# Optimization experiments

Hardware: AMD Instinct MI355X
Metric: run time of the kernel (lower is better)

## Reference

```python
import jax, jax.numpy as jnp
import numpy as np

BCE_W, AMP_W, SMOOTH_W = 1.0, 0.5, 0.3
BIG = 1e30  # finite sentinel for masked min/max (avoids inf-inf NaNs)


def setup_inputs() -> dict:
    key = jax.random.key(0)
    k1, k2, k3 = jax.random.split(key, 3)
    B, L = 128, 100000
    signals = jax.random.normal(k1, (B, 1, L), dtype=jnp.float32)
    predictions = jax.random.normal(k2, (B, L, 1), dtype=jnp.float32)
    targets = jax.random.uniform(k3, (B, L, 1), dtype=jnp.float32)
    return {"signals": signals, "predictions": predictions, "targets": targets}


def _window_amp(mask, s, idx, L):
    # mask: [B, L] bool; s: [B, L] signal. Amplitude of s over [min_idx, max_idx].
    lo = jnp.min(jnp.where(mask, idx, L), axis=1)    # [B]
    hi = jnp.max(jnp.where(mask, idx, -1), axis=1)   # [B]
    w = (idx[None, :] >= lo[:, None]) & (idx[None, :] <= hi[:, None])  # [B, L]
    amp = jnp.max(jnp.where(w, s, -BIG), axis=1) - jnp.min(jnp.where(w, s, BIG), axis=1)
    return amp, jnp.any(mask, axis=1)


def reference(signals, predictions, targets):
    # predictions/targets: [B, L, 1] (3D path of the torch module)
    p, t = predictions, targets
    pred_sigmoid = jax.nn.sigmoid(p)
    # BCEWithLogitsLoss (mean), numerically stable
    bce_loss = jnp.mean(jnp.maximum(p, 0.0) - p * t + jnp.log1p(jnp.exp(-jnp.abs(p))))

    B, L = signals.shape[0], signals.shape[2]
    s = signals[:, 0, :]                              # [B, L]
    idx = jnp.arange(L)

    true_amp, t_has = _window_amp(t[:, :, 0] > 0.5, s, idx, L)
    pred_amp, p_has = _window_amp(pred_sigmoid[:, :, 0] > 0.5, s, idx, L)
    valid = t_has & p_has

    d = jnp.abs(true_amp - pred_amp)
    per = jnp.where(true_amp > 1e-6, d / (true_amp + 1e-6), d)
    amp_loss = jnp.sum(jnp.where(valid, per, 0.0)) / B

    # smoothness: mean |diff(pred_sigmoid, axis=1)|; L >= 2 so never empty
    smoothness_loss = jnp.mean(jnp.abs(pred_sigmoid[:, 1:, :] - pred_sigmoid[:, :-1, :]))

    return BCE_W * bce_loss + AMP_W * amp_loss + SMOOTH_W * smoothness_loss
```

## Files before the change

### kernel.cpp

```cpp
#include <hip/hip_runtime.h>
#include <math.h>
#include <float.h>

#define BATCH 128
#define LEN   100000
#define CHUNK 5000
#define SEGS  (LEN / CHUNK)
#define VPS   (CHUNK / 4)
#define THREADS 512
#define NG    3

struct WS {
    int*   lt_tab; int* ht_tab; int* lp_tab; int* hp_tab;
    float* bce_blk; float* sm_blk;
    float* cmin; float* cmax;
    float* wmn; float* wmx;
};

static inline WS ws_layout(void* d_ws) {
    WS w;
    w.lt_tab  = (int*)d_ws;
    w.ht_tab  = w.lt_tab + BATCH * SEGS;
    w.lp_tab  = w.ht_tab + BATCH * SEGS;
    w.hp_tab  = w.lp_tab + BATCH * SEGS;
    w.bce_blk = (float*)(w.hp_tab + BATCH * SEGS);
    w.sm_blk  = w.bce_blk + BATCH * SEGS;
    w.cmin    = w.sm_blk  + BATCH * SEGS;
    w.cmax    = w.cmin    + BATCH * SEGS;
    w.wmn     = w.cmax    + BATCH * SEGS;
    w.wmx     = w.wmn     + 2 * BATCH;
    return w;
}


__global__ __launch_bounds__(THREADS) void k_main(
        const float* __restrict__ sig,
        const float* __restrict__ pred,
        const float* __restrict__ targ,
        int* __restrict__ lt_tab, int* __restrict__ ht_tab,
        int* __restrict__ lp_tab, int* __restrict__ hp_tab,
        float* __restrict__ bce_blk, float* __restrict__ sm_blk,
        float* __restrict__ cmin_tab, float* __restrict__ cmax_tab) {
    const int b   = blockIdx.y;
    const int seg = blockIdx.x;
    const int tid = threadIdx.x;
    const size_t row = (size_t)b * LEN;
    const float* prow = pred + row;
    const float* trow = targ + row;
    const float* srow = sig  + row;
    const int seg0 = seg * CHUNK;
    const bool g2 = (tid < (VPS - 2 * THREADS));

    float4 pv[NG], tv[NG], sv[NG];
    #pragma unroll
    for (int k = 0; k < NG; ++k) {
        if (k < NG - 1 || g2) {
            const int l0 = seg0 + (tid + k * THREADS) * 4;
            pv[k] = *reinterpret_cast<const float4*>(prow + l0);
            tv[k] = *reinterpret_cast<const float4*>(trow + l0);
            sv[k] = *reinterpret_cast<const float4*>(srow + l0);
        }
    }

    float bce = 0.0f, sm = 0.0f;
    float cmn = FLT_MAX, cmx = -FLT_MAX;
    unsigned tmask = 0u, pmask = 0u;

    #pragma unroll
    for (int k = 0; k < NG; ++k) {
        if (k == NG - 1 && !g2) continue;
        const float4 p4 = pv[k];
        const float4 t4 = tv[k];
        const float4 s4 = sv[k];
        const int l0 = seg0 + (tid + k * THREADS) * 4;
        float sg0, sg1, sg2, sg3;
        #define ONE_ELEM(pp, tt, ss, sgv, BIT) { \
            const float ap = fabsf(pp); \
            const float ee = __expf(-ap); \
            const float zz = 1.0f + ee; \
            const float rr = __builtin_amdgcn_rcpf(zz); \
            bce += fmaxf(pp, 0.0f) - (pp) * (tt) + __logf(zz); \
            sgv = ((pp) >= 0.0f) ? rr : ee * rr; \
            tmask |= ((tt) > 0.5f) ? (1u << (BIT)) : 0u; \
            pmask |= ((pp) > 0.0f) ? (1u << (BIT)) : 0u; \
            cmn = fminf(cmn, (ss)); cmx = fmaxf(cmx, (ss)); }
        ONE_ELEM(p4.x, t4.x, s4.x, sg0, 4 * k + 0)
        ONE_ELEM(p4.y, t4.y, s4.y, sg1, 4 * k + 1)
        ONE_ELEM(p4.z, t4.z, s4.z, sg2, 4 * k + 2)
        ONE_ELEM(p4.w, t4.w, s4.w, sg3, 4 * k + 3)
        #undef ONE_ELEM
        sm += fabsf(sg1 - sg0) + fabsf(sg2 - sg1) + fabsf(sg3 - sg2);
        const float prev3 = __shfl_up(sg3, 1);
        if ((tid & 63) == 0) {
            if (l0 > 0) {
                const float pp = prow[l0 - 1];
                const float ee = __expf(-fabsf(pp));
                const float rr = __builtin_amdgcn_rcpf(1.0f + ee);
                const float sp = (pp >= 0.0f) ? rr : ee * rr;
                sm += fabsf(sg0 - sp);
            }
        } else {
            sm += fabsf(sg0 - prev3);
        }
    }

    int lt = LEN, ht = -1, lp = LEN, hp = -1;
    if (tmask) {
        const int f = __ffs(tmask) - 1;
        const int h = 31 - __clz((int)tmask);
        lt = seg0 + (tid + (f >> 2) * THREADS) * 4 + (f & 3);
        ht = seg0 + (tid + (h >> 2) * THREADS) * 4 + (h & 3);
    }
    if (pmask) {
        const int f = __ffs(pmask) - 1;
        const int h = 31 - __clz((int)pmask);
        lp = seg0 + (tid + (f >> 2) * THREADS) * 4 + (f & 3);
        hp = seg0 + (tid + (h >> 2) * THREADS) * 4 + (h & 3);
    }

    #pragma unroll
    for (int o = 32; o > 0; o >>= 1) {
        bce += __shfl_xor(bce, o);
        sm  += __shfl_xor(sm,  o);
        cmn  = fminf(cmn, __shfl_xor(cmn, o));
        cmx  = fmaxf(cmx, __shfl_xor(cmx, o));
        lt   = min(lt, __shfl_xor(lt, o));
        ht   = max(ht, __shfl_xor(ht, o));
        lp   = min(lp, __shfl_xor(lp, o));
        hp   = max(hp, __shfl_xor(hp, o));
    }

    __shared__ float s_bce[8], s_sm[8], s_mn[8], s_mx[8];
    __shared__ int   s_lt[8], s_ht[8], s_lp[8], s_hp[8];
    const int w = tid >> 6, lane = tid & 63;
    if (lane == 0) {
        s_bce[w] = bce; s_sm[w] = sm; s_mn[w] = cmn; s_mx[w] = cmx;
        s_lt[w] = lt; s_ht[w] = ht; s_lp[w] = lp; s_hp[w] = hp;
    }
    __syncthreads();
    if (tid == 0) {
        float B = 0.0f, S = 0.0f, MN = FLT_MAX, MX = -FLT_MAX;
        int LT = LEN, HT = -1, LP = LEN, HP = -1;
        #pragma unroll
        for (int i = 0; i < 8; ++i) {
            B += s_bce[i]; S += s_sm[i];
            MN = fminf(MN, s_mn[i]); MX = fmaxf(MX, s_mx[i]);
            LT = min(LT, s_lt[i]); HT = max(HT, s_ht[i]);
            LP = min(LP, s_lp[i]); HP = max(HP, s_hp[i]);
        }
        const int e = b * SEGS + seg;
        bce_blk[e] = B; sm_blk[e] = S;
        cmin_tab[e] = MN; cmax_tab[e] = MX;
        lt_tab[e] = LT; ht_tab[e] = HT;
        lp_tab[e] = LP; hp_tab[e] = HP;
    }
}


__global__ __launch_bounds__(THREADS) void k_rows(
        const float* __restrict__ sig,
        const int* __restrict__ lt_tab, const int* __restrict__ ht_tab,
        const int* __restrict__ lp_tab, const int* __restrict__ hp_tab,
        const float* __restrict__ cmin_tab, const float* __restrict__ cmax_tab,
        float* __restrict__ wmn, float* __restrict__ wmx) {
    const int b     = blockIdx.x;
    const int which = blockIdx.y;
    const int tid   = threadIdx.x;
    const int* lo_tab = which ? lp_tab : lt_tab;
    const int* hi_tab = which ? hp_tab : ht_tab;

    int lo = LEN, hi = -1;
    if (tid < SEGS) { lo = lo_tab[b * SEGS + tid]; hi = hi_tab[b * SEGS + tid]; }
    #pragma unroll
    for (int o = 32; o > 0; o >>= 1) {
        lo = min(lo, __shfl_xor(lo, o));
        hi = max(hi, __shfl_xor(hi, o));
    }
    __shared__ int s_lo, s_hi;
    if (tid == 0) { s_lo = lo; s_hi = hi; }
    __syncthreads();
    lo = s_lo; hi = s_hi;

    float mn = FLT_MAX, mx = -FLT_MAX;
    if (lo < LEN) {
        const float* srow = sig + (size_t)b * LEN;
        const int cl = lo / CHUNK, ch = hi / CHUNK;
        const int e1 = (cl == ch) ? hi : cl * CHUNK + CHUNK - 1;
        for (int l = lo + tid; l <= e1; l += THREADS) {
            const float x = srow[l]; mn = fminf(mn, x); mx = fmaxf(mx, x);
        }
        if (ch > cl) {
            for (int l = ch * CHUNK + tid; l <= hi; l += THREADS) {
                const float x = srow[l]; mn = fminf(mn, x); mx = fmaxf(mx, x);
            }
            const float* cmin_row = cmin_tab + b * SEGS;
            const float* cmax_row = cmax_tab + b * SEGS;
            for (int c = cl + 1 + tid; c < ch; c += THREADS) {
                mn = fminf(mn, cmin_row[c]); mx = fmaxf(mx, cmax_row[c]);
            }
        }
    }
    #pragma unroll
    for (int o = 32; o > 0; o >>= 1) {
        mn = fminf(mn, __shfl_xor(mn, o));
        mx = fmaxf(mx, __shfl_xor(mx, o));
    }
    __shared__ float sh_mn[8], sh_mx[8];
    const int w = tid >> 6, lane = tid & 63;
    if (lane == 0) { sh_mn[w] = mn; sh_mx[w] = mx; }
    __syncthreads();
    if (tid == 0) {
        float MN = FLT_MAX, MX = -FLT_MAX;
        #pragma unroll
        for (int i = 0; i < 8; ++i) {
            MN = fminf(MN, sh_mn[i]); MX = fmaxf(MX, sh_mx[i]);
        }
        if (lo >= LEN) { MN = 1e30f; MX = -1e30f; }
        wmn[which * BATCH + b] = MN;
        wmx[which * BATCH + b] = MX;
    }
}


__global__ void k_combine(const float* __restrict__ bce_blk,
                          const float* __restrict__ sm_blk,
                          const float* __restrict__ wmn,
                          const float* __restrict__ wmx,
                          float* __restrict__ out) {
    const int tid = threadIdx.x;
    float acc_b = 0.0f, acc_s = 0.0f, acc_a = 0.0f;
    for (int i = tid; i < BATCH * SEGS; i += 256) { acc_b += bce_blk[i]; acc_s += sm_blk[i]; }
    if (tid < BATCH) {
        const float tmn = wmn[tid],          tmx = wmx[tid];
        const float pmn = wmn[BATCH + tid],  pmx = wmx[BATCH + tid];
        if (tmx >= tmn && pmx >= pmn) {
            const float ta = tmx - tmn;
            const float pa = pmx - pmn;
            const float d  = fabsf(ta - pa);
            acc_a = (ta > 1e-6f) ? d / (ta + 1e-6f) : d;
        }
    }
    #pragma unroll
    for (int o = 32; o > 0; o >>= 1) {
        acc_b += __shfl_xor(acc_b, o);
        acc_s += __shfl_xor(acc_s, o);
        acc_a += __shfl_xor(acc_a, o);
    }
    __shared__ float sb[4], ss[4], sa[4];
    const int w = tid >> 6, lane = tid & 63;
    if (lane == 0) { sb[w] = acc_b; ss[w] = acc_s; sa[w] = acc_a; }
    __syncthreads();
    if (tid == 0) {
        const double B = (double)(sb[0] + sb[1] + sb[2] + sb[3]);
        const double S = (double)(ss[0] + ss[1] + ss[2] + ss[3]);
        const double A = (double)(sa[0] + sa[1] + sa[2] + sa[3]);
        const double bce = B / ((double)BATCH * (double)LEN);
        const double smo = S / ((double)BATCH * (double)(LEN - 1));
        const double amp = A / (double)BATCH;
        out[0] = (float)(1.0 * bce + 0.5 * amp + 0.3 * smo);
    }
}


extern "C" void kernel_launch(void* const* d_in, const int* in_sizes, int n_in,
                              void* d_out, int out_size, void* d_ws, size_t ws_size,
                              hipStream_t stream) {
    const float* signals = (const float*)d_in[0];
    const float* preds   = (const float*)d_in[1];
    const float* targs   = (const float*)d_in[2];
    float* out = (float*)d_out;
    WS w = ws_layout(d_ws);

    dim3 gm(SEGS, BATCH);
    k_main<<<gm, THREADS, 0, stream>>>(signals, preds, targs,
                                       w.lt_tab, w.ht_tab, w.lp_tab, w.hp_tab,
                                       w.bce_blk, w.sm_blk, w.cmin, w.cmax);

    dim3 gr(BATCH, 2);
    k_rows<<<gr, THREADS, 0, stream>>>(signals,
                                       w.lt_tab, w.ht_tab, w.lp_tab, w.hp_tab,
                                       w.cmin, w.cmax, w.wmn, w.wmx);

    k_combine<<<1, 256, 0, stream>>>(w.bce_blk, w.sm_blk, w.wmn, w.wmx, out);
}
```

Baseline: 43.29 us.

## Use fewer larger blocks per row with per-stripe min/max tables

The main kernel now uses 8 blocks per row, each covering 12500 elements over 7 strided iterations, instead of 20 blocks of 5000. Each iteration does its load and compute immediately rather than preloading all groups into registers. Each block records a signal min/max per 2048-element stripe, so the window kernel only rescans the partial boundary stripes instead of whole 5000-element chunks. The grid drops from 2560 to 1024 blocks and the boundary scans get shorter, at the cost of less memory-level parallelism per thread and a 1024-block grid that may underfill the GPU.

```diff
diff --git a/kernel.cpp b/kernel.cpp
--- a/kernel.cpp
+++ b/kernel.cpp
@@ -4,11 +4,17 @@
 
 #define BATCH 128
 #define LEN   100000
-#define CHUNK 5000
-#define SEGS  (LEN / CHUNK)
-#define VPS   (CHUNK / 4)
-#define THREADS 512
-#define NG    3
+#define BPR   8
+#define BCHUNK (LEN / BPR)
+#define BVEC  (BCHUNK / 4)
+#define T     512
+#define NG    7
+#define TAILV (BVEC - (NG - 1) * T)
+#define NST   7
+#define STRE  (T * 4)
+#define TAILE (TAILV * 4)
+#define NSEG  (BATCH * BPR)
+#define NSTR  (NSEG * NST)
 
 struct WS {
     int*   lt_tab; int* ht_tab; int* lp_tab; int* hp_tab;
@@ -20,20 +26,20 @@
 static inline WS ws_layout(void* d_ws) {
     WS w;
     w.lt_tab  = (int*)d_ws;
-    w.ht_tab  = w.lt_tab + BATCH * SEGS;
-    w.lp_tab  = w.ht_tab + BATCH * SEGS;
-    w.hp_tab  = w.lp_tab + BATCH * SEGS;
-    w.bce_blk = (float*)(w.hp_tab + BATCH * SEGS);
-    w.sm_blk  = w.bce_blk + BATCH * SEGS;
-    w.cmin    = w.sm_blk  + BATCH * SEGS;
-    w.cmax    = w.cmin    + BATCH * SEGS;
-    w.wmn     = w.cmax    + BATCH * SEGS;
+    w.ht_tab  = w.lt_tab + NSEG;
+    w.lp_tab  = w.ht_tab + NSEG;
+    w.hp_tab  = w.lp_tab + NSEG;
+    w.bce_blk = (float*)(w.hp_tab + NSEG);
+    w.sm_blk  = w.bce_blk + NSEG;
+    w.cmin    = w.sm_blk  + NSEG;
+    w.cmax    = w.cmin    + NSTR;
+    w.wmn     = w.cmax    + NSTR;
     w.wmx     = w.wmn     + 2 * BATCH;
     return w;
 }
 
 
-__global__ __launch_bounds__(THREADS) void k_main(
+__global__ __launch_bounds__(T, 8) void k_main(
         const float* __restrict__ sig,
         const float* __restrict__ pred,
         const float* __restrict__ targ,
@@ -42,122 +48,140 @@
         float* __restrict__ bce_blk, float* __restrict__ sm_blk,
         float* __restrict__ cmin_tab, float* __restrict__ cmax_tab) {
     const int b   = blockIdx.y;
-    const int seg = blockIdx.x;
+    const int blk = blockIdx.x;
     const int tid = threadIdx.x;
     const size_t row = (size_t)b * LEN;
     const float* prow = pred + row;
     const float* trow = targ + row;
     const float* srow = sig  + row;
-    const int seg0 = seg * CHUNK;
-    const bool g2 = (tid < (VPS - 2 * THREADS));
-
-    float4 pv[NG], tv[NG], sv[NG];
+    const int base = blk * BCHUNK;
+    const int w = tid >> 6, lane = tid & 63;
+
+    __shared__ float s_stmn[8][NST], s_stmx[8][NST];
+    __shared__ float s_bce[8], s_sm[8];
+    __shared__ int   s_lt[8], s_ht[8], s_lp[8], s_hp[8];
+
+    float bce = 0.0f, sm = 0.0f;
+    unsigned tmask = 0u, pmask = 0u;
+
     #pragma unroll
     for (int k = 0; k < NG; ++k) {
-        if (k < NG - 1 || g2) {
-            const int l0 = seg0 + (tid + k * THREADS) * 4;
-            pv[k] = *reinterpret_cast<const float4*>(prow + l0);
-            tv[k] = *reinterpret_cast<const float4*>(trow + l0);
-            sv[k] = *reinterpret_cast<const float4*>(srow + l0);
-        }
-    }
-
-    float bce = 0.0f, sm = 0.0f;
-    float cmn = FLT_MAX, cmx = -FLT_MAX;
-    unsigned tmask = 0u, pmask = 0u;
-
-    #pragma unroll
-    for (int k = 0; k < NG; ++k) {
-        if (k == NG - 1 && !g2) continue;
-        const float4 p4 = pv[k];
-        const float4 t4 = tv[k];
-        const float4 s4 = sv[k];
-        const int l0 = seg0 + (tid + k * THREADS) * 4;
-        float sg0, sg1, sg2, sg3;
-        #define ONE_ELEM(pp, tt, ss, sgv, BIT) { \
-            const float ap = fabsf(pp); \
-            const float ee = __expf(-ap); \
-            const float zz = 1.0f + ee; \
-            const float rr = __builtin_amdgcn_rcpf(zz); \
-            bce += fmaxf(pp, 0.0f) - (pp) * (tt) + __logf(zz); \
-            sgv = ((pp) >= 0.0f) ? rr : ee * rr; \
-            tmask |= ((tt) > 0.5f) ? (1u << (BIT)) : 0u; \
-            pmask |= ((pp) > 0.0f) ? (1u << (BIT)) : 0u; \
-            cmn = fminf(cmn, (ss)); cmx = fmaxf(cmx, (ss)); }
-        ONE_ELEM(p4.x, t4.x, s4.x, sg0, 4 * k + 0)
-        ONE_ELEM(p4.y, t4.y, s4.y, sg1, 4 * k + 1)
-        ONE_ELEM(p4.z, t4.z, s4.z, sg2, 4 * k + 2)
-        ONE_ELEM(p4.w, t4.w, s4.w, sg3, 4 * k + 3)
-        #undef ONE_ELEM
-        sm += fabsf(sg1 - sg0) + fabsf(sg2 - sg1) + fabsf(sg3 - sg2);
-        const float prev3 = __shfl_up(sg3, 1);
-        if ((tid & 63) == 0) {
-            if (l0 > 0) {
-                const float pp = prow[l0 - 1];
-                const float ee = __expf(-fabsf(pp));
-                const float rr = __builtin_amdgcn_rcpf(1.0f + ee);
-                const float sp = (pp >= 0.0f) ? rr : ee * rr;
-                sm += fabsf(sg0 - sp);
+        const bool act = (k < NG - 1) || (tid < TAILV);
+        float gmn = FLT_MAX, gmx = -FLT_MAX;
+        if (act) {
+            const int l0 = base + (tid + k * T) * 4;
+            const float4 p4 = *reinterpret_cast<const float4*>(prow + l0);
+            const float4 t4 = *reinterpret_cast<const float4*>(trow + l0);
+            const float4 s4 = *reinterpret_cast<const float4*>(srow + l0);
+            float sg0, sg1, sg2, sg3;
+            #define ONE_ELEM(pp, tt, ss, sgv, BIT) { \
+                const float ap = fabsf(pp); \
+                const float ee = __expf(-ap); \
+                const float zz = 1.0f + ee; \
+                const float rr = __builtin_amdgcn_rcpf(zz); \
+                bce += fmaxf(pp, 0.0f) - (pp) * (tt) + __logf(zz); \
+                sgv = ((pp) >= 0.0f) ? rr : ee * rr; \
+                tmask |= ((tt) > 0.5f) ? (1u << (BIT)) : 0u; \
+                pmask |= ((pp) > 0.0f) ? (1u << (BIT)) : 0u; \
+                gmn = fminf(gmn, (ss)); gmx = fmaxf(gmx, (ss)); }
+            ONE_ELEM(p4.x, t4.x, s4.x, sg0, 4 * k + 0)
+            ONE_ELEM(p4.y, t4.y, s4.y, sg1, 4 * k + 1)
+            ONE_ELEM(p4.z, t4.z, s4.z, sg2, 4 * k + 2)
+            ONE_ELEM(p4.w, t4.w, s4.w, sg3, 4 * k + 3)
+            #undef ONE_ELEM
+            sm += fabsf(sg1 - sg0) + fabsf(sg2 - sg1) + fabsf(sg3 - sg2);
+            const float prev3 = __shfl_up(sg3, 1);
+            if (lane == 0) {
+                if (l0 > 0) {
+                    const float pp = prow[l0 - 1];
+                    const float ee = __expf(-fabsf(pp));
+                    const float rr = __builtin_amdgcn_rcpf(1.0f + ee);
+                    const float sp = (pp >= 0.0f) ? rr : ee * rr;
+                    sm += fabsf(sg0 - sp);
+                }
+            } else {
+                sm += fabsf(sg0 - prev3);
             }
-        } else {
-            sm += fabsf(sg0 - prev3);
-        }
+        }
+        #pragma unroll
+        for (int o = 32; o > 0; o >>= 1) {
+            gmn = fminf(gmn, __shfl_xor(gmn, o));
+            gmx = fmaxf(gmx, __shfl_xor(gmx, o));
+        }
+        if (lane == 0) { s_stmn[w][k] = gmn; s_stmx[w][k] = gmx; }
     }
 
     int lt = LEN, ht = -1, lp = LEN, hp = -1;
     if (tmask) {
         const int f = __ffs(tmask) - 1;
         const int h = 31 - __clz((int)tmask);
-        lt = seg0 + (tid + (f >> 2) * THREADS) * 4 + (f & 3);
-        ht = seg0 + (tid + (h >> 2) * THREADS) * 4 + (h & 3);
+        lt = base + (tid + (f >> 2) * T) * 4 + (f & 3);
+        ht = base + (tid + (h >> 2) * T) * 4 + (h & 3);
     }
     if (pmask) {
         const int f = __ffs(pmask) - 1;
         const int h = 31 - __clz((int)pmask);
-        lp = seg0 + (tid + (f >> 2) * THREADS) * 4 + (f & 3);
-        hp = seg0 + (tid + (h >> 2) * THREADS) * 4 + (h & 3);
+        lp = base + (tid + (f >> 2) * T) * 4 + (f & 3);
+        hp = base + (tid + (h >> 2) * T) * 4 + (h & 3);
     }
 
     #pragma unroll
     for (int o = 32; o > 0; o >>= 1) {
         bce += __shfl_xor(bce, o);
         sm  += __shfl_xor(sm,  o);
-        cmn  = fminf(cmn, __shfl_xor(cmn, o));
-        cmx  = fmaxf(cmx, __shfl_xor(cmx, o));
         lt   = min(lt, __shfl_xor(lt, o));
         ht   = max(ht, __shfl_xor(ht, o));
         lp   = min(lp, __shfl_xor(lp, o));
         hp   = max(hp, __shfl_xor(hp, o));
     }
-
-    __shared__ float s_bce[8], s_sm[8], s_mn[8], s_mx[8];
-    __shared__ int   s_lt[8], s_ht[8], s_lp[8], s_hp[8];
-    const int w = tid >> 6, lane = tid & 63;
     if (lane == 0) {
-        s_bce[w] = bce; s_sm[w] = sm; s_mn[w] = cmn; s_mx[w] = cmx;
+        s_bce[w] = bce; s_sm[w] = sm;
         s_lt[w] = lt; s_ht[w] = ht; s_lp[w] = lp; s_hp[w] = hp;
     }
     __syncthreads();
+
+    const int e = b * BPR + blk;
     if (tid == 0) {
-        float B = 0.0f, S = 0.0f, MN = FLT_MAX, MX = -FLT_MAX;
+        float B = 0.0f, S = 0.0f;
         int LT = LEN, HT = -1, LP = LEN, HP = -1;
         #pragma unroll
         for (int i = 0; i < 8; ++i) {
             B += s_bce[i]; S += s_sm[i];
-            MN = fminf(MN, s_mn[i]); MX = fmaxf(MX, s_mx[i]);
             LT = min(LT, s_lt[i]); HT = max(HT, s_ht[i]);
             LP = min(LP, s_lp[i]); HP = max(HP, s_hp[i]);
         }
-        const int e = b * SEGS + seg;
         bce_blk[e] = B; sm_blk[e] = S;
-        cmin_tab[e] = MN; cmax_tab[e] = MX;
         lt_tab[e] = LT; ht_tab[e] = HT;
         lp_tab[e] = LP; hp_tab[e] = HP;
     }
-}
-
-
-__global__ __launch_bounds__(THREADS) void k_rows(
+    if (tid < NST) {
+        float mn = s_stmn[0][tid], mx = s_stmx[0][tid];
+        #pragma unroll
+        for (int i = 1; i < 8; ++i) {
+            mn = fminf(mn, s_stmn[i][tid]); mx = fmaxf(mx, s_stmx[i][tid]);
+        }
+        cmin_tab[e * NST + tid] = mn;
+        cmax_tab[e * NST + tid] = mx;
+    }
+}
+
+
+__device__ __forceinline__ int stripe_id(int l) {
+    const int bk = l / BCHUNK;
+    const int rem = l - bk * BCHUNK;
+    int st = rem / STRE;
+    return bk * NST + st;
+}
+__device__ __forceinline__ int stripe_start(int sid) {
+    const int bk = sid / NST, st = sid - bk * NST;
+    return bk * BCHUNK + st * STRE;
+}
+__device__ __forceinline__ int stripe_end(int sid) {
+    const int bk = sid / NST, st = sid - bk * NST;
+    return bk * BCHUNK + st * STRE + ((st < NST - 1) ? STRE : TAILE) - 1;
+}
+
+__global__ __launch_bounds__(T) void k_rows(
         const float* __restrict__ sig,
         const int* __restrict__ lt_tab, const int* __restrict__ ht_tab,
         const int* __restrict__ lp_tab, const int* __restrict__ hp_tab,
@@ -170,7 +194,7 @@
     const int* hi_tab = which ? hp_tab : ht_tab;
 
     int lo = LEN, hi = -1;
-    if (tid < SEGS) { lo = lo_tab[b * SEGS + tid]; hi = hi_tab[b * SEGS + tid]; }
+    if (tid < BPR) { lo = lo_tab[b * BPR + tid]; hi = hi_tab[b * BPR + tid]; }
     #pragma unroll
     for (int o = 32; o > 0; o >>= 1) {
         lo = min(lo, __shfl_xor(lo, o));
@@ -184,19 +208,19 @@
     float mn = FLT_MAX, mx = -FLT_MAX;
     if (lo < LEN) {
         const float* srow = sig + (size_t)b * LEN;
-        const int cl = lo / CHUNK, ch = hi / CHUNK;
-        const int e1 = (cl == ch) ? hi : cl * CHUNK + CHUNK - 1;
-        for (int l = lo + tid; l <= e1; l += THREADS) {
+        const int sl = stripe_id(lo), sh = stripe_id(hi);
+        const int e1 = (sl == sh) ? hi : stripe_end(sl);
+        for (int l = lo + tid; l <= e1; l += T) {
             const float x = srow[l]; mn = fminf(mn, x); mx = fmaxf(mx, x);
         }
-        if (ch > cl) {
-            for (int l = ch * CHUNK + tid; l <= hi; l += THREADS) {
+        if (sh > sl) {
+            for (int l = stripe_start(sh) + tid; l <= hi; l += T) {
                 const float x = srow[l]; mn = fminf(mn, x); mx = fmaxf(mx, x);
             }
-            const float* cmin_row = cmin_tab + b * SEGS;
-            const float* cmax_row = cmax_tab + b * SEGS;
-            for (int c = cl + 1 + tid; c < ch; c += THREADS) {
-                mn = fminf(mn, cmin_row[c]); mx = fmaxf(mx, cmax_row[c]);
+            const float* cmin_row = cmin_tab + b * BPR * NST;
+            const float* cmax_row = cmax_tab + b * BPR * NST;
+            for (int s = sl + 1 + tid; s < sh; s += T) {
+                mn = fminf(mn, cmin_row[s]); mx = fmaxf(mx, cmax_row[s]);
             }
         }
     }
@@ -229,7 +253,7 @@
                           float* __restrict__ out) {
     const int tid = threadIdx.x;
     float acc_b = 0.0f, acc_s = 0.0f, acc_a = 0.0f;
-    for (int i = tid; i < BATCH * SEGS; i += 256) { acc_b += bce_blk[i]; acc_s += sm_blk[i]; }
+    for (int i = tid; i < NSEG; i += 256) { acc_b += bce_blk[i]; acc_s += sm_blk[i]; }
     if (tid < BATCH) {
         const float tmn = wmn[tid],          tmx = wmx[tid];
         const float pmn = wmn[BATCH + tid],  pmx = wmx[BATCH + tid];
@@ -271,15 +295,15 @@
     float* out = (float*)d_out;
     WS w = ws_layout(d_ws);
 
-    dim3 gm(SEGS, BATCH);
-    k_main<<<gm, THREADS, 0, stream>>>(signals, preds, targs,
-                                       w.lt_tab, w.ht_tab, w.lp_tab, w.hp_tab,
-                                       w.bce_blk, w.sm_blk, w.cmin, w.cmax);
+    dim3 gm(BPR, BATCH);
+    k_main<<<gm, T, 0, stream>>>(signals, preds, targs,
+                                 w.lt_tab, w.ht_tab, w.lp_tab, w.hp_tab,
+                                 w.bce_blk, w.sm_blk, w.cmin, w.cmax);
 
     dim3 gr(BATCH, 2);
-    k_rows<<<gr, THREADS, 0, stream>>>(signals,
-                                       w.lt_tab, w.ht_tab, w.lp_tab, w.hp_tab,
-                                       w.cmin, w.cmax, w.wmn, w.wmx);
+    k_rows<<<gr, T, 0, stream>>>(signals,
+                                 w.lt_tab, w.ht_tab, w.lp_tab, w.hp_tab,
+                                 w.cmin, w.cmax, w.wmn, w.wmx);
 
     k_combine<<<1, 256, 0, stream>>>(w.bce_blk, w.sm_blk, w.wmn, w.wmx, out);
 }
```

Result: slower. 59.90 us (+38.4%).
